# Kernel optimization log

Hardware: AMD Instinct MI355X
Metric: run time of the kernel (lower is better)

## Reference

```python
import jax, jax.numpy as jnp
import numpy as np

DIM = 192
HEADS = 8
B, H, W = 2, 256, 256
CPH = DIM // HEADS  # 24 channels per head
EPS = 1e-12

_SOB_DX = np.array([[1, 0, 1], [-2, 0, 2], [-1, 0, 1]], np.float32)
_SOB_DY = np.array([[1, -2, -1], [0, 0, 0], [1, 2, 1]], np.float32)


def _conv2d(x, w, pad, groups=1):
    return jax.lax.conv_general_dilated(
        x, w, window_strides=(1, 1), padding=[(pad, pad), (pad, pad)],
        dimension_numbers=('NCHW', 'OIHW', 'NCHW'), feature_group_count=groups)


def _l2norm(t):
    n = jnp.sqrt(jnp.sum(t * t, axis=-1, keepdims=True))
    return t / jnp.maximum(n, EPS)


def _topk_masked_softmax(attn, k):
    # attn: [B, HEADS, C, C]; keep top-k entries per row, softmax over them.
    b, h, c, _ = attn.shape
    idx = jax.lax.top_k(attn, k)[1]                      # [B,H,C,k]
    flat_idx = idx.reshape(-1, k)
    rows = jnp.arange(flat_idx.shape[0])[:, None]
    mask = jnp.zeros((b * h * c, c), bool).at[rows, flat_idx].set(True)
    masked = jnp.where(mask.reshape(attn.shape), attn, -jnp.inf)
    return jax.nn.softmax(masked, axis=-1)


def setup_inputs() -> dict:
    key = jax.random.key(0)
    ks = jax.random.split(key, 6)
    s = 0.02
    return {
        'x': jax.random.normal(ks[0], (B, DIM, H, W), jnp.float32),
        'q_w': jax.random.normal(ks[1], (DIM, DIM, 1, 1), jnp.float32) * s,
        'q_dw': jax.random.normal(ks[2], (DIM, 1, 3, 3), jnp.float32) * s,
        'kv_w': jax.random.normal(ks[3], (2 * DIM, DIM, 1, 1), jnp.float32) * s,
        'kv_dw': jax.random.normal(ks[4], (2 * DIM, 1, 3, 3), jnp.float32) * s,
        'proj_w': jax.random.normal(ks[5], (DIM, DIM, 1, 1), jnp.float32) * s,
        'temperature': jnp.ones((HEADS, 1, 1), jnp.float32),
        'a1': jnp.full((1,), 0.2, jnp.float32),
        'a2': jnp.full((1,), 0.2, jnp.float32),
        'a3': jnp.full((1,), 0.2, jnp.float32),
        'a4': jnp.full((1,), 0.2, jnp.float32),
    }


def reference(x, q_w, q_dw, kv_w, kv_dw, proj_w, temperature, a1, a2, a3, a4):
    b, c, h, w = x.shape
    # Sob: dense (dim,dim,3,3) Sobel convs (kernel broadcast over all in-channels)
    dx_w = jnp.broadcast_to(jnp.asarray(_SOB_DX), (c, c, 3, 3))
    dy_w = jnp.broadcast_to(jnp.asarray(_SOB_DY), (c, c, 3, 3))
    dx = _conv2d(x, dx_w, 1)
    dy = _conv2d(x, dy_w, 1)

    q_s = _conv2d(_conv2d(dx + dy, q_w, 0), q_dw, 1, groups=c)
    kv = _conv2d(_conv2d(x, kv_w, 0), kv_dw, 1, groups=2 * c)
    k_, v = kv[:, :c], kv[:, c:]

    hw = h * w
    q_s = _l2norm(q_s.reshape(b, HEADS, CPH, hw))
    k_ = _l2norm(k_.reshape(b, HEADS, CPH, hw))
    v = v.reshape(b, HEADS, CPH, hw)

    # channel attention: [B, HEADS, C, C]
    attn = jnp.einsum('bhcn,bhdn->bhcd', q_s, k_) * temperature

    C = CPH
    out = (a1 * (_topk_masked_softmax(attn, int(C / 2)) @ v)
           + a2 * (_topk_masked_softmax(attn, int(C * 2 / 3)) @ v)
           + a3 * (_topk_masked_softmax(attn, int(C * 3 / 4)) @ v)
           + a4 * (_topk_masked_softmax(attn, int(C * 4 / 5)) @ v))

    out = out.reshape(b, c, h, w)
    return _conv2d(out, proj_w, 0)
```

## Files before the change

### kernel.cpp

```cpp
#include <hip/hip_runtime.h>
#include <math.h>

#define NH 8
#define HWv 65536
#define C2 384

typedef __attribute__((ext_vector_type(8))) short bf16x8;
typedef __attribute__((ext_vector_type(4))) float f32x4;

__device__ __forceinline__ float bf2f(unsigned short u) {
    union { unsigned int i; float f; } v; v.i = ((unsigned int)u) << 16; return v.f;
}
__device__ __forceinline__ unsigned short f2bf(float f) {
    union { float f; unsigned int i; } v; v.f = f;
    unsigned int r = v.i + 0x7fff + ((v.i >> 16) & 1);
    return (unsigned short)(r >> 16);
}
__device__ __forceinline__ float hi_of(float a) {
    union { float f; unsigned int i; } u; u.f = a; u.i &= 0xffff0000u; return u.f;
}
__device__ __forceinline__ unsigned short hi16(float a) {
    union { float f; unsigned int i; } u; u.f = a; return (unsigned short)(u.i >> 16);
}
__device__ __forceinline__ unsigned int pack_hi2(float a, float b) {
    union { float f; unsigned int i; } ua, ub; ua.f = a; ub.f = b;
    return (ua.i >> 16) | (ub.i & 0xffff0000u);
}
__device__ __forceinline__ void gld16(const void* g, void* l) {
    __builtin_amdgcn_global_load_lds(
        (const __attribute__((address_space(1))) unsigned int*)g,
        (__attribute__((address_space(3))) unsigned int*)l, 16, 0, 0);
}
__device__ __forceinline__ int rot4(int lb, int row) {
    return (lb + row + (row >> 2)) & 3;
}

__global__ __launch_bounds__(256) void k_wprep(const float* __restrict__ w,
                                               const float* __restrict__ qw,
                                               unsigned short* __restrict__ oh,
                                               unsigned short* __restrict__ ol,
                                               float* __restrict__ qs) {
    if (blockIdx.x == 288) {
        const int o = threadIdx.x;
        if (o < 192) {
            float s = 0.f;
            for (int i = 0; i < 192; ++i) s += qw[(size_t)o * 192 + i];
            qs[o] = s;
        }
        return;
    }
    const int i = blockIdx.x * 256 + threadIdx.x;
    const int e = i & 7, jp = (i >> 3) & 3, rowidx = i >> 5;
    const int o = rowidx % 384, ks = rowidx / 384;
    const int lb = (jp - o - (o >> 2)) & 3;
    const int k = ks * 32 + (lb << 3) + e;
    const float v = w[(size_t)o * 192 + k];
    const unsigned short h = f2bf(v);
    oh[i] = h;
    ol[i] = f2bf(v - bf2f(h));
}

__global__ __launch_bounds__(256, 2) void k_gemm(const float* __restrict__ x,
                                                 const unsigned short* __restrict__ wh,
                                                 const unsigned short* __restrict__ wl,
                                                 unsigned short* __restrict__ t,
                                                 float* __restrict__ s) {
    const int l = blockIdx.x;
    const int xcd = l & 7, idx = l >> 3;
    const int pxtile = xcd * 64 + (idx >> 1);
    const int half = idx & 1;
    const int b = blockIdx.z;
    const int p0 = pxtile * 128;
    const int woff = half * 192;
    const int tid = threadIdx.x;
    const int lane = tid & 63, wv = tid >> 6;
    __shared__ __align__(16) char SU[81920];
    unsigned short* Ts = (unsigned short*)SU;
    float* Ls = (float*)(SU + 26624);
    f32x4 acc[2][12];
#pragma unroll
    for (int m = 0; m < 2; ++m)
#pragma unroll
        for (int n = 0; n < 12; ++n) acc[m][n] = (f32x4){0.f, 0.f, 0.f, 0.f};
    const int px = tid & 127, cg = tid >> 7;
    const float* xb = x + (size_t)b * 192 * HWv + p0 + px;
    const int r = lane & 15, g = lane >> 4;
    const int pbx0 = rot4(2 * cg, px);
    const int pbx1 = rot4(2 * cg + 1, px);
    float csum = 0.f;
    float xr[16];

    auto load_x = [&](int ks) {
#pragma unroll
        for (int i2 = 0; i2 < 8; ++i2) {
            const int c0 = ks * 32 + cg * 16 + i2 * 2;
            xr[2 * i2]     = xb[(size_t)c0 * HWv];
            xr[2 * i2 + 1] = xb[(size_t)(c0 + 1) * HWv];
        }
    };
    auto stage_w = [&](int ks, char* base) {
        const char* gh  = (const char*)wh + ((size_t)(ks * 384 + woff)) * 64;
        const char* gl2 = (const char*)wl + ((size_t)(ks * 384 + woff)) * 64;
        char* lh = base + 16384;
        char* ll = base + 28672;
#pragma unroll
        for (int i = 0; i < 3; ++i) {
            const int chunk = (i * 4 + wv) * 1024;
            gld16(gh + chunk + lane * 16, lh + chunk);
            gld16(gl2 + chunk + lane * 16, ll + chunk);
        }
    };
    auto pack_x = [&](char* base) {
        unsigned short* Xh = (unsigned short*)base;
        unsigned short* Xl = (unsigned short*)(base + 8192);
        unsigned int ph[8], pl[8];
#pragma unroll
        for (int i2 = 0; i2 < 8; ++i2) {
            const float v0 = xr[2 * i2], v1 = xr[2 * i2 + 1];
            csum += v0 + v1;
            ph[i2] = pack_hi2(v0, v1);
            pl[i2] = pack_hi2(v0 - hi_of(v0), v1 - hi_of(v1));
        }
        *(uint4*)&Xh[px * 32 + pbx0 * 8] = make_uint4(ph[0], ph[1], ph[2], ph[3]);
        *(uint4*)&Xh[px * 32 + pbx1 * 8] = make_uint4(ph[4], ph[5], ph[6], ph[7]);
        *(uint4*)&Xl[px * 32 + pbx0 * 8] = make_uint4(pl[0], pl[1], pl[2], pl[3]);
        *(uint4*)&Xl[px * 32 + pbx1 * 8] = make_uint4(pl[4], pl[5], pl[6], pl[7]);
    };

    load_x(0);
    stage_w(0, SU);
    pack_x(SU);
    __syncthreads();

#pragma unroll
    for (int ks = 0; ks < 6; ++ks) {
        char* bc = SU + (ks & 1) * 40960;
        char* bn = SU + ((ks & 1) ^ 1) * 40960;
        if (ks < 5) {
            load_x(ks + 1);
            stage_w(ks + 1, bn);
        }
        unsigned short* Xh  = (unsigned short*)bc;
        unsigned short* Xl  = (unsigned short*)(bc + 8192);
        unsigned short* Whs = (unsigned short*)(bc + 16384);
        unsigned short* Wls = (unsigned short*)(bc + 28672);
        bf16x8 ah[2], al[2];
#pragma unroll
        for (int m = 0; m < 2; ++m) {
            const int row = wv * 32 + m * 16 + r;
            const int ro = rot4(g, row) * 8;
            ah[m] = *(const bf16x8*)&Xh[row * 32 + ro];
            al[m] = *(const bf16x8*)&Xl[row * 32 + ro];
        }
#pragma unroll
        for (int n = 0; n < 12; ++n) {
            const int row = n * 16 + r;
            const int ro = rot4(g, row) * 8;
            const bf16x8 bh = *(const bf16x8*)&Whs[row * 32 + ro];
            const bf16x8 bl = *(const bf16x8*)&Wls[row * 32 + ro];
#pragma unroll
            for (int m = 0; m < 2; ++m) {
                acc[m][n] = __builtin_amdgcn_mfma_f32_16x16x32_bf16(ah[m], bh, acc[m][n], 0, 0, 0);
                acc[m][n] = __builtin_amdgcn_mfma_f32_16x16x32_bf16(ah[m], bl, acc[m][n], 0, 0, 0);
                acc[m][n] = __builtin_amdgcn_mfma_f32_16x16x32_bf16(al[m], bh, acc[m][n], 0, 0, 0);
            }
        }
        if (ks < 5) pack_x(bn);
        __syncthreads();
    }

    if (half == 0) Ls[cg * 128 + px] = csum;
    __syncthreads();
    if (half == 0 && tid < 128)
        s[((size_t)b << 16) + p0 + tid] = Ls[tid] + Ls[128 + tid];
    unsigned short* tb = t + (size_t)b * HWv * C2;
#pragma unroll
    for (int ph2 = 0; ph2 < 2; ++ph2) {
        __syncthreads();
        if ((wv >> 1) == ph2) {
            const int baser = (wv & 1) * 32;
#pragma unroll
            for (int m = 0; m < 2; ++m)
#pragma unroll
                for (int n = 0; n < 12; ++n)
#pragma unroll
                    for (int rr = 0; rr < 4; ++rr)
                        Ts[(baser + m * 16 + g * 4 + rr) * 200 + n * 16 + r] =
                            f2bf(acc[m][n][rr]);
        }
        __syncthreads();
        for (int i = tid; i < 1536; i += 256) {
            const int pxl = i / 24, cho = (i % 24) * 8;
            unsigned short* dst = tb + (size_t)(p0 + ph2 * 64 + pxl) * C2 + woff + cho;
            *(uint4*)dst = *(const uint4*)&Ts[pxl * 200 + cho];
        }
    }
}

__global__ __launch_bounds__(256) void k_attn(const unsigned short* __restrict__ t,
                                              const float* __restrict__ sbuf,
                                              const float* __restrict__ qsum,
                                              const float* __restrict__ qdw,
                                              const float* __restrict__ kvdw,
                                              float* __restrict__ part) {
    const int z = blockIdx.z, b = z >> 3, h = z & 7;
    const int tid = threadIdx.x;
    const int lane = tid & 63, wv = tid >> 6;
    __shared__ __align__(16) char U[50688];
    float* ehalo = (float*)U;
    float* Thalo = (float*)(U + 1296);
    float* shalo = (float*)(U + 32496);
    unsigned short* QKh = (unsigned short*)U;
    unsigned short* QKl = QKh + 48 * 264;
    float* Pp = (float*)U;
    __shared__ float qdwl[216], kdwl[216], qsml[24];
    for (int i = tid; i < 456; i += 256) {
        if (i < 216) qdwl[i] = qdw[h * 216 + i];
        else if (i < 432) kdwl[i - 216] = kvdw[h * 216 + (i - 216)];
        else qsml[i - 432] = qsum[h * 24 + (i - 432)];
    }
    f32x4 acc[6];
#pragma unroll
    for (int tl = 0; tl < 6; ++tl) acc[tl] = (f32x4){0.f, 0.f, 0.f, 0.f};
    const int lr = tid >> 4, lc = tid & 15;
    const int r = lane & 15, g = lane >> 4;
    for (int st = 0; st < 4; ++st) {
        const int tx0 = (blockIdx.x * 2 + (st & 1)) * 16;
        const int ty0 = (blockIdx.y * 2 + (st >> 1)) * 16;
        __syncthreads();
        for (int i = tid; i < 400; i += 256) {
            const int rr = i / 20, cc = i % 20;
            const int y = ty0 - 2 + rr, xx = tx0 - 2 + cc;
            shalo[i] = (y >= 0 && y < 256 && xx >= 0 && xx < 256)
                           ? sbuf[((size_t)b << 16) + y * 256 + xx] : 0.f;
        }
        for (int i = tid; i < 972; i += 256) {
            const int p = i / 3, seg = i % 3;
            const int rr = p / 18, cc = p % 18;
            const int y = ty0 - 1 + rr, xx = tx0 - 1 + cc;
            if (y >= 0 && y < 256 && xx >= 0 && xx < 256) {
                const unsigned short* src =
                    t + ((size_t)b * HWv + y * 256 + xx) * C2 + h * 24 + seg * 8;
                const uint4 v = *(const uint4*)src;
                Thalo[(seg * 8 + 0) * 325 + p] = bf2f((unsigned short)(v.x & 0xffff));
                Thalo[(seg * 8 + 1) * 325 + p] = bf2f((unsigned short)(v.x >> 16));
                Thalo[(seg * 8 + 2) * 325 + p] = bf2f((unsigned short)(v.y & 0xffff));
                Thalo[(seg * 8 + 3) * 325 + p] = bf2f((unsigned short)(v.y >> 16));
                Thalo[(seg * 8 + 4) * 325 + p] = bf2f((unsigned short)(v.z & 0xffff));
                Thalo[(seg * 8 + 5) * 325 + p] = bf2f((unsigned short)(v.z >> 16));
                Thalo[(seg * 8 + 6) * 325 + p] = bf2f((unsigned short)(v.w & 0xffff));
                Thalo[(seg * 8 + 7) * 325 + p] = bf2f((unsigned short)(v.w >> 16));
            } else {
#pragma unroll
                for (int j = 0; j < 8; ++j) Thalo[(seg * 8 + j) * 325 + p] = 0.f;
            }
        }
        __syncthreads();
        for (int i = tid; i < 324; i += 256) {
            const int rr = i / 18, cc = i % 18;
            const int y = ty0 - 1 + rr, xx = tx0 - 1 + cc;
            const float v = (((((shalo[rr * 20 + cc]
                              - shalo[rr * 20 + cc + 1])
                              - shalo[(rr + 1) * 20 + cc])
                              + shalo[(rr + 1) * 20 + cc + 2])
                              + shalo[(rr + 2) * 20 + cc + 1])
                              + shalo[(rr + 2) * 20 + cc + 2]);
            ehalo[i] = (y >= 0 && y < 256 && xx >= 0 && xx < 256) ? 2.f * v : 0.f;
        }
        __syncthreads();
        float qreg[24], kreg[24];
#pragma unroll
        for (int c = 0; c < 24; ++c) {
            float aq = 0.f, ak = 0.f;
#pragma unroll
            for (int dy = 0; dy < 3; ++dy)
#pragma unroll
                for (int dx = 0; dx < 3; ++dx) {
                    aq = fmaf(qdwl[c * 9 + dy * 3 + dx], ehalo[(lr + dy) * 18 + lc + dx], aq);
                    ak = fmaf(kdwl[c * 9 + dy * 3 + dx], Thalo[c * 325 + (lr + dy) * 18 + lc + dx], ak);
                }
            qreg[c] = qsml[c] * aq;
            kreg[c] = ak;
        }
        __syncthreads();
#pragma unroll
        for (int c = 0; c < 24; ++c) {
            const float q = qreg[c], kv = kreg[c];
            QKh[c * 264 + tid] = hi16(q);
            QKl[c * 264 + tid] = hi16(q - hi_of(q));
            QKh[(24 + c) * 264 + tid] = hi16(kv);
            QKl[(24 + c) * 264 + tid] = hi16(kv - hi_of(kv));
        }
        __syncthreads();
#pragma unroll
        for (int c2 = 0; c2 < 2; ++c2) {
            const int colb = (wv * 2 + c2) * 32 + g * 8;
            bf16x8 fh[3], fl[3];
#pragma unroll
            for (int rt = 0; rt < 3; ++rt) {
                fh[rt] = *(const bf16x8*)&QKh[(rt * 16 + r) * 264 + colb];
                fl[rt] = *(const bf16x8*)&QKl[(rt * 16 + r) * 264 + colb];
            }
#define GRAM(T, A, B) \
    acc[T] = __builtin_amdgcn_mfma_f32_16x16x32_bf16(fh[A], fh[B], acc[T], 0, 0, 0); \
    acc[T] = __builtin_amdgcn_mfma_f32_16x16x32_bf16(fh[A], fl[B], acc[T], 0, 0, 0); \
    acc[T] = __builtin_amdgcn_mfma_f32_16x16x32_bf16(fl[A], fh[B], acc[T], 0, 0, 0);
            GRAM(0, 0, 0) GRAM(1, 0, 1) GRAM(2, 0, 2)
            GRAM(3, 1, 1) GRAM(4, 1, 2) GRAM(5, 2, 2)
#undef GRAM
        }
    }
    __syncthreads();
#pragma unroll
    for (int tl = 0; tl < 6; ++tl)
#pragma unroll
        for (int reg = 0; reg < 4; ++reg)
            Pp[wv * 1536 + tl * 256 + (g * 4 + reg) * 16 + r] = acc[tl][reg];
    __syncthreads();
    float* dst = part + ((size_t)z * 64 + blockIdx.y * 8 + blockIdx.x) * 1536;
    for (int i = tid; i < 1536; i += 256)
        dst[i] = Pp[i] + Pp[1536 + i] + Pp[3072 + i] + Pp[4608 + i];
}

__device__ __forceinline__ int gidx(int i, int j) {
    const int rt = i >> 4, ct = j >> 4;
    const int tl = (rt == 0) ? ct : (rt == 1 ? 2 + ct : 5);
    return tl * 256 + (i & 15) * 16 + (j & 15);
}

__global__ __launch_bounds__(256) void k_redcomb(const float* __restrict__ part,
                                                 const float* __restrict__ temp,
                                                 const float* __restrict__ a1,
                                                 const float* __restrict__ a2,
                                                 const float* __restrict__ a3,
                                                 const float* __restrict__ a4,
                                                 float* __restrict__ Wg) {
    const int z = blockIdx.x, b = z >> 3, h = z & 7;
    const int tid = threadIdx.x;
    __shared__ float S[1536];
    __shared__ float att[24][24];
    __shared__ float nq[24], nk[24];
    for (int i = tid; i < 1536; i += 256) {
        float sum = 0.f;
        const float* p = part + (size_t)z * 64 * 1536 + i;
        for (int blk = 0; blk < 64; ++blk) sum += p[(size_t)blk * 1536];
        S[i] = sum;
    }
    __syncthreads();
    if (tid < 24) nq[tid] = fmaxf(sqrtf(S[gidx(tid, tid)]), 1e-12f);
    else if (tid >= 32 && tid < 56) {
        const int d = tid - 32;
        nk[d] = fmaxf(sqrtf(S[gidx(24 + d, 24 + d)]), 1e-12f);
    }
    __syncthreads();
    const float tp = temp[h];
    for (int op = tid; op < 576; op += 256) {
        const int c = op / 24, d = op % 24;
        att[c][d] = S[gidx(c, 24 + d)] * tp / (nq[c] * nk[d]);
    }
    __syncthreads();
    if (tid < 24) {
        const int c = tid;
        float v[24];
#pragma unroll
        for (int d = 0; d < 24; ++d) v[d] = att[c][d];
        int rank[24];
#pragma unroll
        for (int d = 0; d < 24; ++d) {
            int rr = 0;
#pragma unroll
            for (int d2 = 0; d2 < 24; ++d2)
                rr += (v[d2] > v[d]) || (v[d2] == v[d] && d2 < d);
            rank[d] = rr;
        }
        const int ks[4] = {12, 16, 18, 19};
        const float as[4] = {a1[0], a2[0], a3[0], a4[0]};
        float w[24] = {};
        for (int ti = 0; ti < 4; ++ti) {
            const int kk = ks[ti];
            float m = -1e30f;
            for (int d = 0; d < 24; ++d) if (rank[d] < kk) m = fmaxf(m, v[d]);
            float Z = 0.f, ex[24];
            for (int d = 0; d < 24; ++d) {
                ex[d] = (rank[d] < kk) ? expf(v[d] - m) : 0.f;
                Z += ex[d];
            }
            const float sc = as[ti] / Z;
            for (int d = 0; d < 24; ++d) w[d] += ex[d] * sc;
        }
        for (int d = 0; d < 24; ++d)
            Wg[(((size_t)b * NH + h) * 24 + c) * 24 + d] = w[d];
    }
}

__global__ void k_makeM(const float* __restrict__ projw, const float* __restrict__ Wg,
                        unsigned short* __restrict__ Mh, unsigned short* __restrict__ Ml) {
    const int b = blockIdx.x / 192, o = blockIdx.x % 192;
    const int j = threadIdx.x;
    const int h = j / 24, d = j % 24;
    float s = 0.f;
#pragma unroll
    for (int cc = 0; cc < 24; ++cc)
        s = fmaf(projw[(size_t)o * 192 + h * 24 + cc],
                 Wg[(((size_t)b * NH + h) * 24 + cc) * 24 + d], s);
    const unsigned short hh = f2bf(s);
    const int jg = j >> 5, jb = (j >> 3) & 3, e = j & 7;
    const int jp = rot4(jb, o);
    const size_t dst = (((size_t)b * 6 + jg) * 192 + o) * 32 + jp * 8 + e;
    Mh[dst] = hh;
    Ml[dst] = f2bf(s - bf2f(hh));
}

__global__ __launch_bounds__(256) void k_final(const unsigned short* __restrict__ t,
                                               const float* __restrict__ kvdw,
                                               const unsigned short* __restrict__ Mh,
                                               const unsigned short* __restrict__ Ml,
                                               float* __restrict__ out) {
    const int b = blockIdx.y;
    const int tile = blockIdx.x;
    const int x0 = (tile & 15) * 16, y0 = (tile >> 4) * 4;
    const int tid = threadIdx.x;
    const int lane = tid & 63, wv = tid >> 6;
    __shared__ __align__(16) unsigned short Th[108][40];
    __shared__ __align__(16) unsigned short Msh[192 * 32], Msl[192 * 32];
    __shared__ __align__(16) unsigned short Vsh[64][40], Vsl[64][40];
    __shared__ float Wdl[288];
    f32x4 acc[3][4];
#pragma unroll
    for (int m = 0; m < 3; ++m)
#pragma unroll
        for (int n = 0; n < 4; ++n) acc[m][n] = (f32x4){0.f, 0.f, 0.f, 0.f};
    const int px = tid & 63, jq = tid >> 6;
    const int lx = px & 15, ly = px >> 4;
    const int r = lane & 15, g = lane >> 4;
    for (int jg = 0; jg < 6; ++jg) {
        const int j0 = jg * 32;
        __syncthreads();
        {
            const char* gh  = (const char*)Mh + (((size_t)b * 6 + jg) * 192) * 64;
            const char* gl2 = (const char*)Ml + (((size_t)b * 6 + jg) * 192) * 64;
            char* lh = (char*)Msh;
            char* ll = (char*)Msl;
#pragma unroll
            for (int i = 0; i < 3; ++i) {
                const int chunk = (i * 4 + wv) * 1024;
                gld16(gh + chunk + lane * 16, lh + chunk);
                gld16(gl2 + chunk + lane * 16, ll + chunk);
            }
        }
        if (tid < 216) {
            const int hp = tid >> 1, half = tid & 1;
            const int hy = hp / 18, hx = hp % 18;
            const int y = y0 - 1 + hy, xx = x0 - 1 + hx;
            uint4 v0 = make_uint4(0, 0, 0, 0), v1 = make_uint4(0, 0, 0, 0);
            if (y >= 0 && y < 256 && xx >= 0 && xx < 256) {
                const unsigned short* src =
                    t + ((size_t)b * HWv + y * 256 + xx) * C2 + 192 + j0 + half * 16;
                v0 = *(const uint4*)src;
                v1 = *(const uint4*)(src + 8);
            }
            *(uint4*)&Th[hp][half * 16] = v0;
            *(uint4*)&Th[hp][half * 16 + 8] = v1;
        }
        for (int i = tid; i < 288; i += 256) Wdl[i] = kvdw[1728 + jg * 288 + i];
        __syncthreads();
        {
            float vv[8] = {0.f, 0.f, 0.f, 0.f, 0.f, 0.f, 0.f, 0.f};
#pragma unroll
            for (int dy = 0; dy < 3; ++dy)
#pragma unroll
                for (int dx = 0; dx < 3; ++dx) {
                    const int hp = (ly + dy) * 18 + lx + dx;
                    const uint4 tv = *(const uint4*)&Th[hp][jq * 8];
                    float tf[8];
                    tf[0] = bf2f((unsigned short)(tv.x & 0xffff));
                    tf[1] = bf2f((unsigned short)(tv.x >> 16));
                    tf[2] = bf2f((unsigned short)(tv.y & 0xffff));
                    tf[3] = bf2f((unsigned short)(tv.y >> 16));
                    tf[4] = bf2f((unsigned short)(tv.z & 0xffff));
                    tf[5] = bf2f((unsigned short)(tv.z >> 16));
                    tf[6] = bf2f((unsigned short)(tv.w & 0xffff));
                    tf[7] = bf2f((unsigned short)(tv.w >> 16));
                    const int tap = dy * 3 + dx;
#pragma unroll
                    for (int jj = 0; jj < 8; ++jj)
                        vv[jj] = fmaf(Wdl[(jq * 8 + jj) * 9 + tap], tf[jj], vv[jj]);
                }
            unsigned int ph[4], pl[4];
#pragma unroll
            for (int i2 = 0; i2 < 4; ++i2) {
                const float a = vv[i2 * 2], c = vv[i2 * 2 + 1];
                ph[i2] = pack_hi2(a, c);
                pl[i2] = pack_hi2(a - hi_of(a), c - hi_of(c));
            }
            *(uint4*)&Vsh[px][jq * 8] = make_uint4(ph[0], ph[1], ph[2], ph[3]);
            *(uint4*)&Vsl[px][jq * 8] = make_uint4(pl[0], pl[1], pl[2], pl[3]);
        }
        __syncthreads();
        bf16x8 bh[4], bl[4];
#pragma unroll
        for (int n = 0; n < 4; ++n) {
            bh[n] = *(const bf16x8*)&Vsh[n * 16 + r][g * 8];
            bl[n] = *(const bf16x8*)&Vsl[n * 16 + r][g * 8];
        }
#pragma unroll
        for (int m = 0; m < 3; ++m) {
            const int row = wv * 48 + m * 16 + r;
            const int ro = rot4(g, row) * 8;
            const bf16x8 ah = *(const bf16x8*)&Msh[row * 32 + ro];
            const bf16x8 al = *(const bf16x8*)&Msl[row * 32 + ro];
#pragma unroll
            for (int n = 0; n < 4; ++n) {
                acc[m][n] = __builtin_amdgcn_mfma_f32_16x16x32_bf16(ah, bh[n], acc[m][n], 0, 0, 0);
                acc[m][n] = __builtin_amdgcn_mfma_f32_16x16x32_bf16(ah, bl[n], acc[m][n], 0, 0, 0);
                acc[m][n] = __builtin_amdgcn_mfma_f32_16x16x32_bf16(al, bh[n], acc[m][n], 0, 0, 0);
            }
        }
    }
#pragma unroll
    for (int m = 0; m < 3; ++m) {
        const int o = wv * 48 + m * 16 + g * 4;
#pragma unroll
        for (int n = 0; n < 4; ++n) {
            const int p = (y0 + n) * 256 + x0 + r;
#pragma unroll
            for (int rr = 0; rr < 4; ++rr)
                out[((size_t)b * 192 + o + rr) * HWv + p] = acc[m][n][rr];
        }
    }
}


extern "C" void kernel_launch(void* const* d_in, const int* in_sizes, int n_in,
                              void* d_out, int out_size, void* d_ws, size_t ws_size,
                              hipStream_t stream) {
    (void)in_sizes; (void)n_in; (void)out_size;
    const float* x     = (const float*)d_in[0];
    const float* qw    = (const float*)d_in[1];
    const float* qdw   = (const float*)d_in[2];
    const float* kvw   = (const float*)d_in[3];
    const float* kvdw  = (const float*)d_in[4];
    const float* projw = (const float*)d_in[5];
    const float* temp  = (const float*)d_in[6];
    const float* a1    = (const float*)d_in[7];
    const float* a2    = (const float*)d_in[8];
    const float* a3    = (const float*)d_in[9];
    const float* a4    = (const float*)d_in[10];
    float* out = (float*)d_out;

    const size_t T_EL = (size_t)2 * HWv * C2;
    const size_t needB = T_EL * 2
                       + (size_t)(131072 + 131072 + 192 + 1572864 + 24576 + 9216) * 4
                       + (size_t)(73728 * 4) * 2;
    if (ws_size < needB) return;
    unsigned short* t = (unsigned short*)d_ws;
    float* s    = (float*)(t + T_EL);
    float* e    = s + 131072;
    float* qsum = e + 131072;
    float* part = qsum + 192;
    float* accS = part + 1572864;
    float* Wg   = accS + 24576;
    unsigned short* wh = (unsigned short*)(Wg + 9216);
    unsigned short* wl = wh + 73728;
    unsigned short* Mh = wl + 73728;
    unsigned short* Ml = Mh + 73728;

    k_wprep<<<289, 256, 0, stream>>>(kvw, qw, wh, wl, qsum);
    k_gemm<<<dim3(1024, 1, 2), 256, 0, stream>>>(x, wh, wl, t, s);
    k_attn<<<dim3(8, 8, 16), 256, 0, stream>>>(t, s, qsum, qdw, kvdw, part);
    k_redcomb<<<16, 256, 0, stream>>>(part, temp, a1, a2, a3, a4, Wg);
    k_makeM<<<384, 192, 0, stream>>>(projw, Wg, Mh, Ml);
    k_final<<<dim3(1024, 2), 256, 0, stream>>>(t, kvdw, Mh, Ml, out);
}
```

Measured before the change: 263.7 us.

## Single-buffer X tile and double-buffer only weights in GEMM LDS pipeline

Restructures the k-loop of the 1x1-conv GEMM kernel. X is no longer prefetched into registers and double-buffered in LDS. Each iteration now loads X, packs it into a single LDS buffer, and synchronises with explicit barriers, while only the weight tiles keep async double-buffering. This cuts shared memory from 80 KB to 64 KB, which should make it easier to fit two blocks per CU. The cost is that the global X loads are exposed on every step instead of overlapping with the MFMA work.

```diff
diff --git a/kernel.cpp b/kernel.cpp
--- a/kernel.cpp
+++ b/kernel.cpp
@@ -74,7 +74,9 @@
     const int woff = half * 192;
     const int tid = threadIdx.x;
     const int lane = tid & 63, wv = tid >> 6;
-    __shared__ __align__(16) char SU[81920];
+    __shared__ __align__(16) char SU[65536];
+    unsigned short* Xh = (unsigned short*)SU;
+    unsigned short* Xl = (unsigned short*)(SU + 8192);
     unsigned short* Ts = (unsigned short*)SU;
     float* Ls = (float*)(SU + 26624);
     f32x4 acc[2][12];
@@ -88,62 +90,62 @@
     const int pbx0 = rot4(2 * cg, px);
     const int pbx1 = rot4(2 * cg + 1, px);
     float csum = 0.f;
-    float xr[16];
-
-    auto load_x = [&](int ks) {
+
+    {
+        const char* gh  = (const char*)wh + ((size_t)woff) * 64;
+        const char* gl2 = (const char*)wl + ((size_t)woff) * 64;
+        char* wbase = SU + 16384;
+#pragma unroll
+        for (int i = 0; i < 3; ++i) {
+            const int chunk = (i * 4 + wv) * 1024;
+            gld16(gh + chunk + lane * 16, wbase + chunk);
+            gld16(gl2 + chunk + lane * 16, wbase + 12288 + chunk);
+        }
+    }
+
+    for (int ks = 0; ks < 6; ++ks) {
+        __builtin_amdgcn_sched_barrier(0);
+        __builtin_amdgcn_s_barrier();
+        __builtin_amdgcn_sched_barrier(0);
+        float xr[16];
 #pragma unroll
         for (int i2 = 0; i2 < 8; ++i2) {
             const int c0 = ks * 32 + cg * 16 + i2 * 2;
             xr[2 * i2]     = xb[(size_t)c0 * HWv];
             xr[2 * i2 + 1] = xb[(size_t)(c0 + 1) * HWv];
         }
-    };
-    auto stage_w = [&](int ks, char* base) {
-        const char* gh  = (const char*)wh + ((size_t)(ks * 384 + woff)) * 64;
-        const char* gl2 = (const char*)wl + ((size_t)(ks * 384 + woff)) * 64;
-        char* lh = base + 16384;
-        char* ll = base + 28672;
-#pragma unroll
-        for (int i = 0; i < 3; ++i) {
-            const int chunk = (i * 4 + wv) * 1024;
-            gld16(gh + chunk + lane * 16, lh + chunk);
-            gld16(gl2 + chunk + lane * 16, ll + chunk);
-        }
-    };
-    auto pack_x = [&](char* base) {
-        unsigned short* Xh = (unsigned short*)base;
-        unsigned short* Xl = (unsigned short*)(base + 8192);
-        unsigned int ph[8], pl[8];
-#pragma unroll
-        for (int i2 = 0; i2 < 8; ++i2) {
-            const float v0 = xr[2 * i2], v1 = xr[2 * i2 + 1];
-            csum += v0 + v1;
-            ph[i2] = pack_hi2(v0, v1);
-            pl[i2] = pack_hi2(v0 - hi_of(v0), v1 - hi_of(v1));
-        }
-        *(uint4*)&Xh[px * 32 + pbx0 * 8] = make_uint4(ph[0], ph[1], ph[2], ph[3]);
-        *(uint4*)&Xh[px * 32 + pbx1 * 8] = make_uint4(ph[4], ph[5], ph[6], ph[7]);
-        *(uint4*)&Xl[px * 32 + pbx0 * 8] = make_uint4(pl[0], pl[1], pl[2], pl[3]);
-        *(uint4*)&Xl[px * 32 + pbx1 * 8] = make_uint4(pl[4], pl[5], pl[6], pl[7]);
-    };
-
-    load_x(0);
-    stage_w(0, SU);
-    pack_x(SU);
-    __syncthreads();
-
-#pragma unroll
-    for (int ks = 0; ks < 6; ++ks) {
-        char* bc = SU + (ks & 1) * 40960;
-        char* bn = SU + ((ks & 1) ^ 1) * 40960;
+        __builtin_amdgcn_sched_barrier(0);
         if (ks < 5) {
-            load_x(ks + 1);
-            stage_w(ks + 1, bn);
-        }
-        unsigned short* Xh  = (unsigned short*)bc;
-        unsigned short* Xl  = (unsigned short*)(bc + 8192);
-        unsigned short* Whs = (unsigned short*)(bc + 16384);
-        unsigned short* Wls = (unsigned short*)(bc + 28672);
+            const char* gh  = (const char*)wh + ((size_t)((ks + 1) * 384 + woff)) * 64;
+            const char* gl2 = (const char*)wl + ((size_t)((ks + 1) * 384 + woff)) * 64;
+            char* wbase = SU + 16384 + (((ks + 1) & 1) ? 24576 : 0);
+#pragma unroll
+            for (int i = 0; i < 3; ++i) {
+                const int chunk = (i * 4 + wv) * 1024;
+                gld16(gh + chunk + lane * 16, wbase + chunk);
+                gld16(gl2 + chunk + lane * 16, wbase + 12288 + chunk);
+            }
+        }
+        {
+            unsigned int ph[8], pl[8];
+#pragma unroll
+            for (int i2 = 0; i2 < 8; ++i2) {
+                const float v0 = xr[2 * i2], v1 = xr[2 * i2 + 1];
+                csum += v0 + v1;
+                ph[i2] = pack_hi2(v0, v1);
+                pl[i2] = pack_hi2(v0 - hi_of(v0), v1 - hi_of(v1));
+            }
+            *(uint4*)&Xh[px * 32 + pbx0 * 8] = make_uint4(ph[0], ph[1], ph[2], ph[3]);
+            *(uint4*)&Xh[px * 32 + pbx1 * 8] = make_uint4(ph[4], ph[5], ph[6], ph[7]);
+            *(uint4*)&Xl[px * 32 + pbx0 * 8] = make_uint4(pl[0], pl[1], pl[2], pl[3]);
+            *(uint4*)&Xl[px * 32 + pbx1 * 8] = make_uint4(pl[4], pl[5], pl[6], pl[7]);
+        }
+        asm volatile("s_waitcnt lgkmcnt(0)" ::: "memory");
+        __builtin_amdgcn_s_barrier();
+        __builtin_amdgcn_sched_barrier(0);
+        const unsigned short* Whs =
+            (const unsigned short*)(SU + 16384 + ((ks & 1) ? 24576 : 0));
+        const unsigned short* Wls = Whs + 6144;
         bf16x8 ah[2], al[2];
 #pragma unroll
         for (int m = 0; m < 2; ++m) {
@@ -165,10 +167,8 @@
                 acc[m][n] = __builtin_amdgcn_mfma_f32_16x16x32_bf16(al[m], bh, acc[m][n], 0, 0, 0);
             }
         }
-        if (ks < 5) pack_x(bn);
-        __syncthreads();
-    }
-
+    }
+    __syncthreads();
     if (half == 0) Ls[cg * 128 + px] = csum;
     __syncthreads();
     if (half == 0 && tid < 128)
```

Result: no change. 262.0 us (-0.6%).
